# Optimization experiments

Measured on AMD Instinct MI355X. Metric: run time of the kernel, lower is better.

Reference implementation:

```python
import jax, jax.numpy as jnp
import numpy as np


def setup_inputs() -> dict:
    key = jax.random.key(0)
    ks = jax.random.split(key, 5)
    S, B, T = 512, 1024, 64
    emissions = jax.random.normal(ks[0], (S, B, T), dtype=jnp.float32)
    tags = jax.random.randint(ks[1], (S, B), 0, T, dtype=jnp.int64)
    mask = jnp.ones((S, B), dtype=bool)
    start_transitions = jax.random.normal(ks[2], (T,), dtype=jnp.float32)
    end_transitions = jax.random.normal(ks[3], (T,), dtype=jnp.float32)
    # xavier_normal on (T, T): std = sqrt(2 / (T + T))
    transitions = jax.random.normal(ks[4], (T, T), dtype=jnp.float32) * np.sqrt(2.0 / (T + T)).astype(np.float32)
    return {"emissions": emissions, "tags": tags, "mask": mask,
            "start_transitions": start_transitions,
            "end_transitions": end_transitions,
            "transitions": transitions}


def _joint_likelihood(emissions, tags, mask, start_transitions, end_transitions, transitions):
    # emissions: (S, B, T); tags, mask: (S, B)
    S, B, T = emissions.shape
    maskf = mask.astype(emissions.dtype)
    b = jnp.arange(B)
    # transition scores between consecutive tags, masked by next-step mask
    trans_score = transitions[tags[:-1], tags[1:]] * maskf[1:]          # (S-1, B)
    # emission score of current tag at steps 0..S-2, masked by current mask
    emit_score = jnp.take_along_axis(emissions[:-1], tags[:-1, :, None], axis=2)[..., 0] * maskf[:-1]  # (S-1, B)
    last_tag_index = maskf.sum(0).astype(jnp.int32) - 1                 # (B,)
    last_tags = tags[last_tag_index, b]                                 # (B,)
    score = (start_transitions[tags[0]]
             + trans_score.sum(0)
             + emit_score.sum(0)
             + end_transitions[last_tags]
             + emissions[-1, b, last_tags] * maskf[-1])
    return score  # (B,)


def _input_likelihood(emissions, mask, start_transitions, end_transitions, transitions):
    # forward algorithm via lax.scan over time
    alpha0 = start_transitions[None, :] + emissions[0]                  # (B, T)

    def step(alpha, inp):
        emit_i, mask_i = inp                                            # (B, T), (B,)
        # inner: (B, prev_tag, next_tag)
        inner = alpha[:, :, None] + transitions[None, :, :] + emit_i[:, None, :]
        new_alpha = jax.nn.logsumexp(inner, axis=1)                     # (B, T)
        alpha = jnp.where(mask_i[:, None], new_alpha, alpha)
        return alpha, None

    alpha, _ = jax.lax.scan(step, alpha0, (emissions[1:], mask[1:]))
    stops = alpha + end_transitions[None, :]
    return jax.nn.logsumexp(stops, axis=-1)                             # (B,)


def reference(emissions, tags, mask, start_transitions, end_transitions, transitions):
    numerator = _joint_likelihood(emissions, tags, mask, start_transitions, end_transitions, transitions)
    denominator = _input_likelihood(emissions, mask, start_transitions, end_transitions, transitions)
    return jnp.sum(numerator - denominator)
```

## Files before the change

### kernel.cpp

```cpp
#include <hip/hip_runtime.h>


#define S_LEN 512
#define B_SZ  1024
#define T_SZ  64

typedef unsigned uvec2 __attribute__((ext_vector_type(2)));

__global__ void __launch_bounds__(512)
__attribute__((amdgpu_waves_per_eu(2, 2)))
crf_main(const float* __restrict__ emissions,
         const int*   __restrict__ tags,
         const float* __restrict__ start_t,
         const float* __restrict__ end_t,
         const float* __restrict__ trans,
         float*       __restrict__ partial)
{
    __shared__ float Dlds[4][64];
    __shared__ int   eBs[4];
    __shared__ float nBs[4];
    __shared__ float wres[4];

    const int tid  = threadIdx.x;
    const int w    = tid >> 6;
    const int lane = tid & 63;
    const bool fwd = (w < 4);
    const int b    = blockIdx.x * 4 + (w & 3);
    const int g    = lane >> 4;
    const int p    = lane & 15;

    const int probe = __builtin_amdgcn_update_dpp(lane, lane, 0x121, 0xF, 0xF, false);
    const int d = (probe - p) & 15;

#if __has_builtin(__builtin_amdgcn_permlane16_swap)
    const uvec2 pr16 = __builtin_amdgcn_permlane16_swap((unsigned)lane, (unsigned)lane, false, false);
    const bool  m16  = (pr16[0] == (unsigned)(lane ^ 16));
#endif
#if __has_builtin(__builtin_amdgcn_permlane32_swap)
    const uvec2 pr32 = __builtin_amdgcn_permlane32_swap((unsigned)lane, (unsigned)lane, false, false);
    const bool  m32  = (pr32[0] == (unsigned)(lane ^ 32));
#endif

    auto xor16 = [&](float v) -> float {
#if __has_builtin(__builtin_amdgcn_permlane16_swap)
        const unsigned iv = (unsigned)__float_as_int(v);
        const uvec2 r = __builtin_amdgcn_permlane16_swap(iv, iv, false, false);
        return __int_as_float((int)(m16 ? r[0] : r[1]));
#else
        return __int_as_float(__builtin_amdgcn_ds_swizzle(__float_as_int(v), 0x401F));
#endif
    };
    auto xor32 = [&](float v) -> float {
#if __has_builtin(__builtin_amdgcn_permlane32_swap)
        const unsigned iv = (unsigned)__float_as_int(v);
        const uvec2 r = __builtin_amdgcn_permlane32_swap(iv, iv, false, false);
        return __int_as_float((int)(m32 ? r[0] : r[1]));
#else
        return __shfl_xor(v, 32, 64);
#endif
    };

#define EINIT(k, r)                                                          \
    float e##k##_##r; {                                                      \
        const int si_ = (((g) ^ (k)) << 4) | (((p) + (d) * (r)) & 15);       \
        e##k##_##r = __expf(trans[fwd ? (si_ * T_SZ + lane)                  \
                                      : (lane * T_SZ + si_)]);               \
    }
#define EINIT_K(k) \
    EINIT(k, 0)  EINIT(k, 1)  EINIT(k, 2)  EINIT(k, 3)  \
    EINIT(k, 4)  EINIT(k, 5)  EINIT(k, 6)  EINIT(k, 7)  \
    EINIT(k, 8)  EINIT(k, 9)  EINIT(k, 10) EINIT(k, 11) \
    EINIT(k, 12) EINIT(k, 13) EINIT(k, 14) EINIT(k, 15)
    EINIT_K(0) EINIT_K(1) EINIT_K(2) EINIT_K(3)
#undef EINIT_K
#undef EINIT

    const int BT = B_SZ * T_SZ;
    const float* eb = emissions + b * T_SZ + lane;

#define FMAC_DPP(q, c, e, rs)                                            \
    asm("v_fmac_f32_dpp %0, %1, %2 row_ror:" rs " row_mask:0xf bank_mask:0xf" \
        : "+v"(q) : "v"(c), "v"(e));
#define ACC4(r)                          \
    FMAC_DPP(q0, c0v, e0_##r, #r)        \
    FMAC_DPP(q1, c1v, e1_##r, #r)        \
    FMAC_DPP(q2, c2v, e2_##r, #r)        \
    FMAC_DPP(q3, c3v, e3_##r, #r)

    auto core = [&](float c0v) -> float {
        const float c1v = xor16(c0v);
        const float c2v = xor32(c0v);
        const float c3v = xor16(c2v);
        float q0 = c0v * e0_0;
        float q1 = c1v * e1_0;
        float q2 = c2v * e2_0;
        float q3 = c3v * e3_0;
        asm volatile("s_nop 2");
        ACC4(1)  ACC4(2)  ACC4(3)  ACC4(4)  ACC4(5)
        ACC4(6)  ACC4(7)  ACC4(8)  ACC4(9)  ACC4(10)
        ACC4(11) ACC4(12) ACC4(13) ACC4(14) ACC4(15)
        return (q0 + q1) + (q2 + q3);
    };

    auto rescale = [&](float r, int& etot_) -> float {
        const unsigned rb =
            (unsigned)__builtin_amdgcn_readfirstlane(__float_as_int(r));
        const int ex = (int)((rb >> 23) & 0xFFu) - 127;
        etot_ += ex;
        return ldexpf(r, -ex);
    };

    float cur;
    int   etot = 0;
    float ebuf[6];

    if (fwd) {
        cur = __expf(start_t[lane] + eb[0]);
        #pragma unroll
        for (int k = 0; k < 6; ++k) ebuf[k] = eb[(1 + k) * BT];
        float ex = __expf(ebuf[0]);
        for (int it = 0; it < 42; ++it) {
            const int s0 = 1 + it * 6;
            #pragma unroll
            for (int u = 0; u < 6; ++u) {
                ebuf[u] = eb[(s0 + u + 6) * BT];
                const float exn = __expf(ebuf[(u + 1) % 6]);
                const float r = core(cur) * ex;
                ex  = exn;
                cur = (u == 5) ? rescale(r, etot) : r;
            }
        }
        #pragma unroll
        for (int u = 0; u < 4; ++u) {
            const float r = core(cur) * ex;
            ex  = __expf(ebuf[u + 1]);
            cur = r;
        }
        cur = rescale(cur, etot);
    } else {
        cur = __expf(end_t[lane]);
        #pragma unroll
        for (int k = 0; k < 6; ++k) ebuf[k] = eb[(511 - k) * BT];
        float ex = __expf(ebuf[0]);
        for (int it = 0; it < 42; ++it) {
            const int t0 = 511 - it * 6;
            #pragma unroll
            for (int u = 0; u < 6; ++u) {
                ebuf[u] = eb[(t0 - u - 6) * BT];
                const float exn = __expf(ebuf[(u + 1) % 6]);
                const float r = core(cur * ex);
                ex  = exn;
                cur = (u == 5) ? rescale(r, etot) : r;
            }
        }
        #pragma unroll
        for (int u = 0; u < 3; ++u) {
            const float r = core(cur * ex);
            ex  = __expf(ebuf[u + 1]);
            cur = r;
        }
        cur = rescale(cur, etot);
    }

    float nacc = 0.f;
    const int t8lo = fwd ? 0 : 4;
    #pragma unroll
    for (int t8i = 0; t8i < 4; ++t8i) {
        const int s  = (t8lo + t8i) * 64 + lane;
        const int tg = tags[s * B_SZ + b];
        nacc += emissions[(s * B_SZ + b) * T_SZ + tg];
        if (s == 0) nacc += start_t[tg];
        if (s == S_LEN - 1) {
            nacc += end_t[tg];
        } else {
            nacc += trans[tg * T_SZ + tags[(s + 1) * B_SZ + b]];
        }
    }
    #pragma unroll
    for (int m = 1; m < 64; m <<= 1) nacc += __shfl_xor(nacc, m, 64);

    if (!fwd) {
        Dlds[w - 4][lane] = cur;
        if (lane == 0) { eBs[w - 4] = etot; nBs[w - 4] = nacc; }
    }
    __syncthreads();
    if (fwd) {
        float prod = cur * Dlds[w][lane];
        #pragma unroll
        for (int m = 1; m < 64; m <<= 1) prod += __shfl_xor(prod, m, 64);
        const float den = (float)(etot + eBs[w]) * 0.69314718055994530942f
                          + __logf(prod);
        if (lane == 0) wres[w] = (nacc + nBs[w]) - den;
    }
    __syncthreads();
    if (tid == 0)
        partial[blockIdx.x] = (wres[0] + wres[1]) + (wres[2] + wres[3]);
}

__global__ void crf_reduce(const float* __restrict__ partial,
                           float* __restrict__ out)
{
    const int lane = threadIdx.x;
    float s = 0.f;
    #pragma unroll
    for (int k = 0; k < 4; ++k) s += partial[k * 64 + lane];
    #pragma unroll
    for (int m = 1; m < 64; m <<= 1) s += __shfl_xor(s, m, 64);
    if (lane == 0) out[0] = s;
}

extern "C" void kernel_launch(void* const* d_in, const int* in_sizes, int n_in,
                              void* d_out, int out_size, void* d_ws, size_t ws_size,
                              hipStream_t stream)
{
    const float* emissions = (const float*)d_in[0];
    const int*   tags      = (const int*)d_in[1];
    const float* start_t   = (const float*)d_in[3];
    const float* end_t     = (const float*)d_in[4];
    const float* trans     = (const float*)d_in[5];

    float* out     = (float*)d_out;
    float* partial = (float*)d_ws;

    crf_main<<<dim3(256), dim3(512), 0, stream>>>(emissions, tags, start_t,
                                                  end_t, trans, partial);
    crf_reduce<<<dim3(1), dim3(64), 0, stream>>>(partial, out);
}
```

Baseline: 105.0 us.

## Broadcast alpha through LDS float4 reads instead of DPP/permlane cross-lane FMAs

The per-step 64x64 matrix-vector product in the CRF forward/backward recurrence stops using row_ror DPP fused FMAs and permlane swaps to rotate the state across lanes. Each wave now writes its state vector to a shared-memory row and reads it back as 16 broadcast float4 loads, multiplying by 64 register-resident exp(transition) values per lane. This drops the cross-lane shuffle setup and DPP hazard nops in exchange for an LDS write/read round trip on the serial dependency chain every time step. There is no barrier between the write and the reads because each wave uses only its own row.

```diff
diff --git a/kernel.cpp b/kernel.cpp
--- a/kernel.cpp
+++ b/kernel.cpp
@@ -4,8 +4,6 @@
 #define S_LEN 512
 #define B_SZ  1024
 #define T_SZ  64
-
-typedef unsigned uvec2 __attribute__((ext_vector_type(2)));
 
 __global__ void __launch_bounds__(512)
 __attribute__((amdgpu_waves_per_eu(2, 2)))
@@ -16,6 +14,7 @@
          const float* __restrict__ trans,
          float*       __restrict__ partial)
 {
+    __shared__ float pbuf[8][64];
     __shared__ float Dlds[4][64];
     __shared__ int   eBs[4];
     __shared__ float nBs[4];
@@ -26,79 +25,61 @@
     const int lane = tid & 63;
     const bool fwd = (w < 4);
     const int b    = blockIdx.x * 4 + (w & 3);
-    const int g    = lane >> 4;
-    const int p    = lane & 15;
-
-    const int probe = __builtin_amdgcn_update_dpp(lane, lane, 0x121, 0xF, 0xF, false);
-    const int d = (probe - p) & 15;
-
-#if __has_builtin(__builtin_amdgcn_permlane16_swap)
-    const uvec2 pr16 = __builtin_amdgcn_permlane16_swap((unsigned)lane, (unsigned)lane, false, false);
-    const bool  m16  = (pr16[0] == (unsigned)(lane ^ 16));
-#endif
-#if __has_builtin(__builtin_amdgcn_permlane32_swap)
-    const uvec2 pr32 = __builtin_amdgcn_permlane32_swap((unsigned)lane, (unsigned)lane, false, false);
-    const bool  m32  = (pr32[0] == (unsigned)(lane ^ 32));
-#endif
-
-    auto xor16 = [&](float v) -> float {
-#if __has_builtin(__builtin_amdgcn_permlane16_swap)
-        const unsigned iv = (unsigned)__float_as_int(v);
-        const uvec2 r = __builtin_amdgcn_permlane16_swap(iv, iv, false, false);
-        return __int_as_float((int)(m16 ? r[0] : r[1]));
-#else
-        return __int_as_float(__builtin_amdgcn_ds_swizzle(__float_as_int(v), 0x401F));
-#endif
-    };
-    auto xor32 = [&](float v) -> float {
-#if __has_builtin(__builtin_amdgcn_permlane32_swap)
-        const unsigned iv = (unsigned)__float_as_int(v);
-        const uvec2 r = __builtin_amdgcn_permlane32_swap(iv, iv, false, false);
-        return __int_as_float((int)(m32 ? r[0] : r[1]));
-#else
-        return __shfl_xor(v, 32, 64);
-#endif
-    };
-
-#define EINIT(k, r)                                                          \
-    float e##k##_##r; {                                                      \
-        const int si_ = (((g) ^ (k)) << 4) | (((p) + (d) * (r)) & 15);       \
-        e##k##_##r = __expf(trans[fwd ? (si_ * T_SZ + lane)                  \
-                                      : (lane * T_SZ + si_)]);               \
-    }
-#define EINIT_K(k) \
-    EINIT(k, 0)  EINIT(k, 1)  EINIT(k, 2)  EINIT(k, 3)  \
-    EINIT(k, 4)  EINIT(k, 5)  EINIT(k, 6)  EINIT(k, 7)  \
-    EINIT(k, 8)  EINIT(k, 9)  EINIT(k, 10) EINIT(k, 11) \
-    EINIT(k, 12) EINIT(k, 13) EINIT(k, 14) EINIT(k, 15)
-    EINIT_K(0) EINIT_K(1) EINIT_K(2) EINIT_K(3)
-#undef EINIT_K
+
+#define EINIT(i) \
+    float E##i = __expf(trans[fwd ? ((i) * T_SZ + lane) : (lane * T_SZ + (i))]);
+    EINIT(0)  EINIT(1)  EINIT(2)  EINIT(3)  EINIT(4)  EINIT(5)  EINIT(6)  EINIT(7)
+    EINIT(8)  EINIT(9)  EINIT(10) EINIT(11) EINIT(12) EINIT(13) EINIT(14) EINIT(15)
+    EINIT(16) EINIT(17) EINIT(18) EINIT(19) EINIT(20) EINIT(21) EINIT(22) EINIT(23)
+    EINIT(24) EINIT(25) EINIT(26) EINIT(27) EINIT(28) EINIT(29) EINIT(30) EINIT(31)
+    EINIT(32) EINIT(33) EINIT(34) EINIT(35) EINIT(36) EINIT(37) EINIT(38) EINIT(39)
+    EINIT(40) EINIT(41) EINIT(42) EINIT(43) EINIT(44) EINIT(45) EINIT(46) EINIT(47)
+    EINIT(48) EINIT(49) EINIT(50) EINIT(51) EINIT(52) EINIT(53) EINIT(54) EINIT(55)
+    EINIT(56) EINIT(57) EINIT(58) EINIT(59) EINIT(60) EINIT(61) EINIT(62) EINIT(63)
 #undef EINIT
+#define EPIN(i) asm volatile("" : "+v"(E##i));
+    EPIN(0)  EPIN(1)  EPIN(2)  EPIN(3)  EPIN(4)  EPIN(5)  EPIN(6)  EPIN(7)
+    EPIN(8)  EPIN(9)  EPIN(10) EPIN(11) EPIN(12) EPIN(13) EPIN(14) EPIN(15)
+    EPIN(16) EPIN(17) EPIN(18) EPIN(19) EPIN(20) EPIN(21) EPIN(22) EPIN(23)
+    EPIN(24) EPIN(25) EPIN(26) EPIN(27) EPIN(28) EPIN(29) EPIN(30) EPIN(31)
+    EPIN(32) EPIN(33) EPIN(34) EPIN(35) EPIN(36) EPIN(37) EPIN(38) EPIN(39)
+    EPIN(40) EPIN(41) EPIN(42) EPIN(43) EPIN(44) EPIN(45) EPIN(46) EPIN(47)
+    EPIN(48) EPIN(49) EPIN(50) EPIN(51) EPIN(52) EPIN(53) EPIN(54) EPIN(55)
+    EPIN(56) EPIN(57) EPIN(58) EPIN(59) EPIN(60) EPIN(61) EPIN(62) EPIN(63)
+#undef EPIN
 
     const int BT = B_SZ * T_SZ;
     const float* eb = emissions + b * T_SZ + lane;
-
-#define FMAC_DPP(q, c, e, rs)                                            \
-    asm("v_fmac_f32_dpp %0, %1, %2 row_ror:" rs " row_mask:0xf bank_mask:0xf" \
-        : "+v"(q) : "v"(c), "v"(e));
-#define ACC4(r)                          \
-    FMAC_DPP(q0, c0v, e0_##r, #r)        \
-    FMAC_DPP(q1, c1v, e1_##r, #r)        \
-    FMAC_DPP(q2, c2v, e2_##r, #r)        \
-    FMAC_DPP(q3, c3v, e3_##r, #r)
-
-    auto core = [&](float c0v) -> float {
-        const float c1v = xor16(c0v);
-        const float c2v = xor32(c0v);
-        const float c3v = xor16(c2v);
-        float q0 = c0v * e0_0;
-        float q1 = c1v * e1_0;
-        float q2 = c2v * e2_0;
-        float q3 = c3v * e3_0;
-        asm volatile("s_nop 2");
-        ACC4(1)  ACC4(2)  ACC4(3)  ACC4(4)  ACC4(5)
-        ACC4(6)  ACC4(7)  ACC4(8)  ACC4(9)  ACC4(10)
-        ACC4(11) ACC4(12) ACC4(13) ACC4(14) ACC4(15)
+    float* const prow = &pbuf[w][0];
+
+    auto core = [&](float c) -> float {
+        prow[lane] = c;
+        float q0 = 0.f, q1 = 0.f, q2 = 0.f, q3 = 0.f;
+#define MAC4(k, Ea, Eb, Ec, Ed)                                      \
+        {                                                            \
+            const float4 c4 = *reinterpret_cast<const float4*>(prow + 4 * (k)); \
+            q0 = fmaf(c4.x, Ea, q0);                                 \
+            q1 = fmaf(c4.y, Eb, q1);                                 \
+            q2 = fmaf(c4.z, Ec, q2);                                 \
+            q3 = fmaf(c4.w, Ed, q3);                                 \
+        }
+        MAC4(0,  E0,  E1,  E2,  E3)
+        MAC4(1,  E4,  E5,  E6,  E7)
+        MAC4(2,  E8,  E9,  E10, E11)
+        MAC4(3,  E12, E13, E14, E15)
+        MAC4(4,  E16, E17, E18, E19)
+        MAC4(5,  E20, E21, E22, E23)
+        MAC4(6,  E24, E25, E26, E27)
+        MAC4(7,  E28, E29, E30, E31)
+        MAC4(8,  E32, E33, E34, E35)
+        MAC4(9,  E36, E37, E38, E39)
+        MAC4(10, E40, E41, E42, E43)
+        MAC4(11, E44, E45, E46, E47)
+        MAC4(12, E48, E49, E50, E51)
+        MAC4(13, E52, E53, E54, E55)
+        MAC4(14, E56, E57, E58, E59)
+        MAC4(15, E60, E61, E62, E63)
+#undef MAC4
         return (q0 + q1) + (q2 + q3);
     };
 
```

Measured after the change: 96.19 us. -8.4%, faster.

## Replace DPP row-rotate matvec with LDS broadcast and packed FMA

Applied to the files above, without the earlier changes.

The per-step 64x64 matrix-vector product in the CRF recurrence is restructured. Previously each lane held rotated transition entries and used DPP row_ror FMACs plus cross-row swaps. Now each lane writes its alpha value to LDS, reads back a 16-element slice as float4 vectors, and does packed v_pk_fma_f32 against transition pairs. Partial sums are then combined with xor32/xor16 reductions and a select. The aim is to halve FMA instruction count through packed math, at the cost of an LDS round trip and extra cross-lane reduction on every step of the serial chain.

```diff
diff --git a/kernel.cpp b/kernel.cpp
--- a/kernel.cpp
+++ b/kernel.cpp
@@ -5,6 +5,8 @@
 #define B_SZ  1024
 #define T_SZ  64
 
+typedef float f32x4 __attribute__((ext_vector_type(4)));
+typedef float f32x2 __attribute__((ext_vector_type(2)));
 typedef unsigned uvec2 __attribute__((ext_vector_type(2)));
 
 __global__ void __launch_bounds__(512)
@@ -16,6 +18,7 @@
          const float* __restrict__ trans,
          float*       __restrict__ partial)
 {
+    __shared__ float pbuf[8][64];
     __shared__ float Dlds[4][64];
     __shared__ int   eBs[4];
     __shared__ float nBs[4];
@@ -28,9 +31,9 @@
     const int b    = blockIdx.x * 4 + (w & 3);
     const int g    = lane >> 4;
     const int p    = lane & 15;
-
-    const int probe = __builtin_amdgcn_update_dpp(lane, lane, 0x121, 0xF, 0xF, false);
-    const int d = (probe - p) & 15;
+    const int ib   = g << 4;
+    const bool gb0 = (g & 1) != 0;
+    const bool gb1 = (g & 2) != 0;
 
 #if __has_builtin(__builtin_amdgcn_permlane16_swap)
     const uvec2 pr16 = __builtin_amdgcn_permlane16_swap((unsigned)lane, (unsigned)lane, false, false);
@@ -60,46 +63,62 @@
 #endif
     };
 
-#define EINIT(k, r)                                                          \
-    float e##k##_##r; {                                                      \
-        const int si_ = (((g) ^ (k)) << 4) | (((p) + (d) * (r)) & 15);       \
-        e##k##_##r = __expf(trans[fwd ? (si_ * T_SZ + lane)                  \
-                                      : (lane * T_SZ + si_)]);               \
-    }
-#define EINIT_K(k) \
-    EINIT(k, 0)  EINIT(k, 1)  EINIT(k, 2)  EINIT(k, 3)  \
-    EINIT(k, 4)  EINIT(k, 5)  EINIT(k, 6)  EINIT(k, 7)  \
-    EINIT(k, 8)  EINIT(k, 9)  EINIT(k, 10) EINIT(k, 11) \
-    EINIT(k, 12) EINIT(k, 13) EINIT(k, 14) EINIT(k, 15)
-    EINIT_K(0) EINIT_K(1) EINIT_K(2) EINIT_K(3)
-#undef EINIT_K
-#undef EINIT
+#define EE(ii, jj) __expf(trans[fwd ? ((ii) * T_SZ + (jj)) : ((jj) * T_SZ + (ii))])
+#define EPINIT(k, m)                                                        \
+    f32x2 Ea_##k##_##m = { EE(ib + 4 * (k) + 0, 16 * (m) + p),              \
+                           EE(ib + 4 * (k) + 1, 16 * (m) + p) };            \
+    f32x2 Eb_##k##_##m = { EE(ib + 4 * (k) + 2, 16 * (m) + p),              \
+                           EE(ib + 4 * (k) + 3, 16 * (m) + p) };
+#define EPINIT_K(k) EPINIT(k, 0) EPINIT(k, 1) EPINIT(k, 2) EPINIT(k, 3)
+    EPINIT_K(0) EPINIT_K(1) EPINIT_K(2) EPINIT_K(3)
+#undef EPINIT_K
+#undef EPINIT
+#undef EE
+#define EPIN(k, m) asm volatile("" : "+v"(Ea_##k##_##m), "+v"(Eb_##k##_##m));
+#define EPIN_K(k) EPIN(k, 0) EPIN(k, 1) EPIN(k, 2) EPIN(k, 3)
+    EPIN_K(0) EPIN_K(1) EPIN_K(2) EPIN_K(3)
+#undef EPIN_K
+#undef EPIN
 
     const int BT = B_SZ * T_SZ;
     const float* eb = emissions + b * T_SZ + lane;
-
-#define FMAC_DPP(q, c, e, rs)                                            \
-    asm("v_fmac_f32_dpp %0, %1, %2 row_ror:" rs " row_mask:0xf bank_mask:0xf" \
-        : "+v"(q) : "v"(c), "v"(e));
-#define ACC4(r)                          \
-    FMAC_DPP(q0, c0v, e0_##r, #r)        \
-    FMAC_DPP(q1, c1v, e1_##r, #r)        \
-    FMAC_DPP(q2, c2v, e2_##r, #r)        \
-    FMAC_DPP(q3, c3v, e3_##r, #r)
-
-    auto core = [&](float c0v) -> float {
-        const float c1v = xor16(c0v);
-        const float c2v = xor32(c0v);
-        const float c3v = xor16(c2v);
-        float q0 = c0v * e0_0;
-        float q1 = c1v * e1_0;
-        float q2 = c2v * e2_0;
-        float q3 = c3v * e3_0;
-        asm volatile("s_nop 2");
-        ACC4(1)  ACC4(2)  ACC4(3)  ACC4(4)  ACC4(5)
-        ACC4(6)  ACC4(7)  ACC4(8)  ACC4(9)  ACC4(10)
-        ACC4(11) ACC4(12) ACC4(13) ACC4(14) ACC4(15)
-        return (q0 + q1) + (q2 + q3);
+    float* const prow = &pbuf[w][0];
+    const float* const pslice = prow + ib;
+
+#define PKFMA(q, a, e) \
+    asm("v_pk_fma_f32 %0, %1, %2, %0" : "+v"(q) : "v"(a), "v"(e));
+
+    auto core = [&](float c) -> float {
+        prow[lane] = c;
+        f32x2 q0 = {0.f, 0.f}, q1 = {0.f, 0.f};
+        f32x2 q2 = {0.f, 0.f}, q3 = {0.f, 0.f};
+#define CHUNK(k)                                                          \
+        {                                                                 \
+            const f32x4 c4 = *reinterpret_cast<const f32x4*>(pslice + 4 * (k)); \
+            const f32x2 cl = __builtin_shufflevector(c4, c4, 0, 1);       \
+            const f32x2 ch = __builtin_shufflevector(c4, c4, 2, 3);       \
+            PKFMA(q0, cl, Ea_##k##_0) PKFMA(q0, ch, Eb_##k##_0)           \
+            PKFMA(q1, cl, Ea_##k##_1) PKFMA(q1, ch, Eb_##k##_1)           \
+            PKFMA(q2, cl, Ea_##k##_2) PKFMA(q2, ch, Eb_##k##_2)           \
+            PKFMA(q3, cl, Ea_##k##_3) PKFMA(q3, ch, Eb_##k##_3)           \
+        }
+        CHUNK(0) CHUNK(1) CHUNK(2) CHUNK(3)
+#undef CHUNK
+        const float A0 = q0.x + q0.y;
+        const float A1 = q1.x + q1.y;
+        const float A2 = q2.x + q2.y;
+        const float A3 = q3.x + q3.y;
+        const float B0 = A0 + xor32(A0);
+        const float B1 = A1 + xor32(A1);
+        const float B2 = A2 + xor32(A2);
+        const float B3 = A3 + xor32(A3);
+        const float C0 = B0 + xor16(B0);
+        const float C1 = B1 + xor16(B1);
+        const float C2 = B2 + xor16(B2);
+        const float C3 = B3 + xor16(B3);
+        const float s01 = gb0 ? C1 : C0;
+        const float s23 = gb0 ? C3 : C2;
+        return gb1 ? s23 : s01;
     };
 
     auto rescale = [&](float r, int& etot_) -> float {
```

After: 116.5 us. +10.9%, slower.
